# Kernel optimization log

Measured on AMD Instinct MI355X. Metric: run time of the kernel, lower is better.

The kernel has to match this reference:

```python
import jax, jax.numpy as jnp
import numpy as np


def gin_layer(x, src, dst, ew, w1, b1, w2, b2):
    # message: gather source features, scale by edge weight  [E, d]
    msg = x[src] * ew[:, None]
    # scatter-add into destination nodes  [N, d]
    agg = jax.ops.segment_sum(msg, dst, num_segments=x.shape[0])
    # GIN update: (1 + eps) * x + aggregate, eps = 0 (default)
    h = agg + x
    # 2-layer MLP (Linear -> ReLU -> Linear, plain last layer)
    h = jax.nn.relu(h @ w1 + b1)
    return h @ w2 + b2


def setup_inputs() -> dict:
    key = jax.random.key(0)
    ks = jax.random.split(key, 16)
    N, E, D = 100000, 1000000, 64
    x = jax.random.normal(ks[0], (N, D), dtype=jnp.float32)
    edge_index = jax.random.randint(ks[1], (2, E), 0, N)
    edge_weight = jax.random.uniform(ks[2], (E,), dtype=jnp.float32)

    def lin(k, fi, fo):
        return jax.random.normal(k, (fi, fo), dtype=jnp.float32) * (1.0 / np.sqrt(fi))

    return {
        "x": x, "edge_index": edge_index, "edge_weight": edge_weight,
        "w11": lin(ks[3], 64, 64),  "b11": jnp.zeros(64, jnp.float32),
        "w12": lin(ks[4], 64, 64),  "b12": jnp.zeros(64, jnp.float32),
        "w21": lin(ks[5], 64, 128), "b21": jnp.zeros(128, jnp.float32),
        "w22": lin(ks[6], 128, 64), "b22": jnp.zeros(64, jnp.float32),
        "w31": lin(ks[7], 64, 64),  "b31": jnp.zeros(64, jnp.float32),
        "w32": lin(ks[8], 64, 64),  "b32": jnp.zeros(64, jnp.float32),
    }


def reference(x, edge_index, edge_weight,
              w11, b11, w12, b12,
              w21, b21, w22, b22,
              w31, b31, w32, b32):
    src, dst = edge_index[0], edge_index[1]
    # dropout is identity in eval mode
    h = gin_layer(x, src, dst, edge_weight, w11, b11, w12, b12)
    h = jax.nn.relu(h)
    h = gin_layer(h, src, dst, edge_weight, w21, b21, w22, b22)
    h = jax.nn.relu(h)
    h = gin_layer(h, src, dst, edge_weight, w31, b31, w32, b32)
    return h
```

## Files before the change

kernel.cpp:

```cpp
#include <hip/hip_runtime.h>
#include <math.h>


#define FEAT  64
#define BINW  128
#define BSH   7
#define NBLK  256
#define SRCB  25
#define PADSLACK 2048

typedef __attribute__((ext_vector_type(8))) short bfrag;
typedef __attribute__((ext_vector_type(4))) float ffrag;
typedef __attribute__((ext_vector_type(2))) float f32x2;

__device__ __forceinline__ unsigned short f2bf_rne(float x) {
    union { float f; unsigned u; } v; v.f = x;
    unsigned r = (v.u + 0x7fffu + ((v.u >> 16) & 1u)) >> 16;
    return (unsigned short)r;
}
__device__ __forceinline__ float bf2f(unsigned short h) {
    union { unsigned u; float f; } v; v.u = ((unsigned)h) << 16;
    return v.f;
}
__device__ __forceinline__ f32x2 bf2x2(unsigned d) {
    f32x2 r;
    r.x = __uint_as_float(d << 16);
    r.y = __uint_as_float(d & 0xffff0000u);
    return r;
}
__device__ __forceinline__ unsigned cvt_pk_bf16(float a, float b) {
    unsigned r;
    asm("v_cvt_pk_bf16_f32 %0, %1, %2" : "=v"(r) : "v"(a), "v"(b));
    return r;
}
__device__ __forceinline__ void split8(const float u[8], bfrag& hi, bfrag& lo) {
    union { unsigned d[4]; bfrag b; } ch, cl;
#pragma unroll
    for (int i = 0; i < 4; ++i) {
        unsigned h = cvt_pk_bf16(u[2*i], u[2*i+1]);
        float f0 = __uint_as_float(h << 16);
        float f1 = __uint_as_float(h & 0xffff0000u);
        ch.d[i] = h;
        cl.d[i] = cvt_pk_bf16(u[2*i] - f0, u[2*i+1] - f1);
    }
    hi = ch.b; lo = cl.b;
}

__device__ __forceinline__ void pack_one(const float* __restrict__ w,
                                         unsigned short* __restrict__ hi,
                                         unsigned short* __restrict__ lo,
                                         int K, int Hc, int i) {
    int KF = K >> 5;
    int j    = i & 7;
    int lane = (i >> 3) & 63;
    int fb   = i >> 9;
    int kf   = fb % KF;
    int cg   = fb / KF;
    int k    = kf * 32 + ((lane >> 4) << 3) + j;
    int col  = cg * 16 + (lane & 15);
    float x = w[k * Hc + col];
    unsigned short h = f2bf_rne(x);
    hi[i] = h;
    lo[i] = f2bf_rne(x - bf2f(h));
}

__global__ __launch_bounds__(256)
void k_pre(const float4* __restrict__ x4, ushort4* __restrict__ xb4,
           int n4, int gCvt,
           const int* __restrict__ dst, int* __restrict__ counts,
           int E, int NBINS,
           const float* w11, const float* w12, const float* w21,
           const float* w22, const float* w31, const float* w32,
           unsigned short* p11h, unsigned short* p11l,
           unsigned short* p12h, unsigned short* p12l,
           unsigned short* p21h, unsigned short* p21l,
           unsigned short* p22h, unsigned short* p22l,
           unsigned short* p31h, unsigned short* p31l,
           unsigned short* p32h, unsigned short* p32l) {
    __shared__ int h[1024];
    const int bb = blockIdx.x, tid = threadIdx.x;
    if (bb < gCvt) {
        int i = bb * 256 + tid;
        if (i < n4) {
            float4 v = x4[i];
            ushort4 o;
            o.x = f2bf_rne(v.x); o.y = f2bf_rne(v.y);
            o.z = f2bf_rne(v.z); o.w = f2bf_rne(v.w);
            xb4[i] = o;
        }
    } else if (bb < gCvt + NBLK) {
        const int b = bb - gCvt;
        for (int i = tid; i < NBINS; i += 256) h[i] = 0;
        __syncthreads();
        const int chunk = (E + NBLK - 1) / NBLK;
        const int ebeg = b * chunk;
        const int eend = (ebeg + chunk < E) ? ebeg + chunk : E;
        for (int e = ebeg + tid; e < eend; e += 256)
            atomicAdd(&h[dst[e] >> BSH], 1);
        __syncthreads();
        for (int i = tid; i < NBINS; i += 256)
            counts[i * NBLK + b] = h[i];
    } else {
        int i = (bb - gCvt - NBLK) * 256 + tid;
        if      (i <  4096) pack_one(w11, p11h, p11l,  64,  64, i);
        else if (i <  8192) pack_one(w12, p12h, p12l,  64,  64, i - 4096);
        else if (i < 16384) pack_one(w21, p21h, p21l,  64, 128, i - 8192);
        else if (i < 24576) pack_one(w22, p22h, p22l, 128,  64, i - 16384);
        else if (i < 28672) pack_one(w31, p31h, p31l,  64,  64, i - 24576);
        else                pack_one(w32, p32h, p32l,  64,  64, i - 28672);
    }
}

__global__ __launch_bounds__(256)
void k_scanA2(int* __restrict__ counts, int* __restrict__ bintotal, int NBINS) {
    __shared__ int tmp[256];
    const int bin = blockIdx.x, tid = threadIdx.x;
    int c = counts[bin * NBLK + tid];
    tmp[tid] = c;
    __syncthreads();
    for (int off = 1; off < 256; off <<= 1) {
        int t = (tid >= off) ? tmp[tid - off] : 0;
        __syncthreads();
        tmp[tid] += t;
        __syncthreads();
    }
    counts[bin * NBLK + tid] = tmp[tid] - c;
    if (tid == 255) bintotal[bin] = tmp[255];
}

__global__ __launch_bounds__(256)
void k_place2(const int* __restrict__ src, const int* __restrict__ dst,
              const float* __restrict__ ew, const int* __restrict__ counts,
              const int* __restrict__ bintotal, int* __restrict__ binstart,
              int2* __restrict__ binbuf, int E, int NBINS) {
    __shared__ int bs[1024];
    __shared__ int tmp[256];
    __shared__ int base[1024];
    const int b = blockIdx.x, tid = threadIdx.x;

    int v[4]; int s = 0;
#pragma unroll
    for (int j = 0; j < 4; ++j) {
        int idx = tid * 4 + j;
        v[j] = (idx < NBINS) ? bintotal[idx] : 0;
        s += v[j];
    }
    tmp[tid] = s;
    __syncthreads();
    for (int off = 1; off < 256; off <<= 1) {
        int t = (tid >= off) ? tmp[tid - off] : 0;
        __syncthreads();
        tmp[tid] += t;
        __syncthreads();
    }
    int run = tmp[tid] - s;
#pragma unroll
    for (int j = 0; j < 4; ++j) {
        bs[tid * 4 + j] = run;
        run += v[j];
    }
    __syncthreads();

    if (b == 0) {
        for (int i = tid; i < NBINS; i += 256) binstart[i] = bs[i];
        if (tid == 0) binstart[NBINS] = E;
    }

    for (int i = tid; i < NBINS; i += 256)
        base[i] = bs[i] + counts[i * NBLK + b];
    __syncthreads();

    const int chunk = (E + NBLK - 1) / NBLK;
    const int ebeg = b * chunk;
    const int eend = (ebeg + chunk < E) ? ebeg + chunk : E;
    for (int e = ebeg + tid; e < eend; e += 256) {
        int d = dst[e];
        int slot = atomicAdd(&base[d >> BSH], 1);
        int key = ((d & (BINW - 1)) << SRCB) | src[e];
        binbuf[slot] = make_int2(key, __float_as_int(ew[e]));
    }
}

__global__ __launch_bounds__(256)
void k_binsort(const int2* __restrict__ binbuf, const int* __restrict__ binstart,
               int* __restrict__ pbeg, int* __restrict__ pend,
               int2* __restrict__ csr_pad, int N) {
    __shared__ int cnt[BINW];
    __shared__ int cur[BINW];
    __shared__ int pex[BINW];
    const int b    = blockIdx.x;
    const int base = binstart[b];
    const int ne   = binstart[b + 1] - base;
    const int tid  = threadIdx.x;
    const int base_pad = ((base + 15) & ~15) + b * PADSLACK;

    if (tid < BINW) cnt[tid] = 0;
    __syncthreads();
    for (int i = tid; i < ne; i += 256)
        atomicAdd(&cnt[(binbuf[base + i].x >> SRCB) & (BINW - 1)], 1);
    __syncthreads();
    int pc = 0;
    if (tid < BINW) {
        int c = cnt[tid];
        pc = c ? ((c + 15) & ~15) : 16;
        cur[tid] = pc;
    }
    __syncthreads();
    for (int off = 1; off < BINW; off <<= 1) {
        int v = (tid < BINW && tid >= off) ? cur[tid - off] : 0;
        __syncthreads();
        if (tid < BINW) cur[tid] += v;
        __syncthreads();
    }
    if (tid < BINW) {
        int ex = cur[tid] - pc;
        pex[tid] = ex;
        int node = b * BINW + tid;
        if (node < N) {
            pbeg[node] = base_pad + ex;
            pend[node] = base_pad + ex + pc;
        }
        cur[tid] = 0;
    }
    __syncthreads();
    for (int i = tid; i < ne; i += 256) {
        int2 e = binbuf[base + i];
        int dl = (e.x >> SRCB) & (BINW - 1);
        int r = atomicAdd(&cur[dl], 1);
        csr_pad[base_pad + pex[dl] + r] =
            make_int2((e.x & ((1 << SRCB) - 1)) << 7, e.y);
    }
    __syncthreads();
    if (tid < BINW) {
        int c = cnt[tid];
        int pcn = c ? ((c + 15) & ~15) : 16;
        int o = base_pad + pex[tid];
        for (int j = c; j < pcn; ++j)
            csr_pad[o + j] = make_int2(0, 0);
    }
}

template<int H, bool RELU_OUT, bool OUT_BF16>
__global__ __launch_bounds__(256)
void k_fused(const ushort* __restrict__ in, void* __restrict__ outv,
             const int* __restrict__ pbeg, const int* __restrict__ pend,
             const int2* __restrict__ csr_pad,
             const unsigned short* __restrict__ w1h, const unsigned short* __restrict__ w1l,
             const float* __restrict__ b1,
             const unsigned short* __restrict__ w2h, const unsigned short* __restrict__ w2l,
             const float* __restrict__ b2, int N) {
    constexpr int SH   = H + 4;
    constexpr int CG1  = H / 16;
    constexpr int CGH1 = CG1 / 4;
    constexpr int KF2  = H / 32;
    __shared__ float hs[16 * SH];

    const int t = threadIdx.x;
    const int wk = t >> 6, lane = t & 63;
    const int m = lane & 15, q = lane >> 4;
    const int m8 = m * 8;
    const int tnode0 = blockIdx.x * 16;
    float* hw = hs;
    const char* inB = reinterpret_cast<const char*>(in);
    const int4* csr4 = reinterpret_cast<const int4*>(csr_pad);

    const int gnode = tnode0 + wk * 4 + q;
    const int beg = pbeg[gnode];
    const int end = pend[gnode];
    uint2 xr = *reinterpret_cast<const uint2*>(inB + (size_t)gnode * 128 + m8);

    {
        const int nl = wk * 4 + q;
        f32x2 acc01 = {0.f, 0.f};
        f32x2 acc23 = {0.f, 0.f};
        for (int p = beg; p < end; p += 16) {
            int4 e2[8];
#pragma unroll
            for (int u = 0; u < 8; ++u)
                e2[u] = csr4[(p >> 1) + u];
            uint2 v2[16];
#pragma unroll
            for (int u = 0; u < 8; ++u) {
                v2[2*u]   = *reinterpret_cast<const uint2*>(inB + (unsigned)e2[u].x + m8);
                v2[2*u+1] = *reinterpret_cast<const uint2*>(inB + (unsigned)e2[u].z + m8);
            }
#pragma unroll
            for (int u = 0; u < 8; ++u) {
                f32x2 w0 = {__int_as_float(e2[u].y), __int_as_float(e2[u].y)};
                f32x2 w1 = {__int_as_float(e2[u].w), __int_as_float(e2[u].w)};
                acc01 = __builtin_elementwise_fma(w0, bf2x2(v2[2*u].x),   acc01);
                acc23 = __builtin_elementwise_fma(w0, bf2x2(v2[2*u].y),   acc23);
                acc01 = __builtin_elementwise_fma(w1, bf2x2(v2[2*u+1].x), acc01);
                acc23 = __builtin_elementwise_fma(w1, bf2x2(v2[2*u+1].y), acc23);
            }
        }
        acc01 = acc01 + bf2x2(xr.x);
        acc23 = acc23 + bf2x2(xr.y);
        float4 accv = make_float4(acc01.x, acc01.y, acc23.x, acc23.y);
        *reinterpret_cast<float4*>(&hw[nl * SH + m * 4]) = accv;
    }
    __syncthreads();

    const bfrag* w1hp = reinterpret_cast<const bfrag*>(w1h);
    const bfrag* w1lp = reinterpret_cast<const bfrag*>(w1l);
    const bfrag* w2hp = reinterpret_cast<const bfrag*>(w2h);
    const bfrag* w2lp = reinterpret_cast<const bfrag*>(w2l);

    bfrag ah[2], al[2];
#pragma unroll
    for (int kf = 0; kf < 2; ++kf) {
        const float* base = &hw[m * SH + kf * 32 + q * 8];
        float4 u0 = *reinterpret_cast<const float4*>(base);
        float4 u1 = *reinterpret_cast<const float4*>(base + 4);
        float u[8] = {u0.x, u0.y, u0.z, u0.w, u1.x, u1.y, u1.z, u1.w};
        split8(u, ah[kf], al[kf]);
    }
    __syncthreads();

    __builtin_amdgcn_s_setprio(1);
#pragma unroll
    for (int cgi = 0; cgi < CGH1; ++cgi) {
        const int cg = wk * CGH1 + cgi;
        ffrag c = {0.f, 0.f, 0.f, 0.f};
#pragma unroll
        for (int kf = 0; kf < 2; ++kf) {
            bfrag bh = w1hp[(cg * 2 + kf) * 64 + lane];
            bfrag bl = w1lp[(cg * 2 + kf) * 64 + lane];
            c = __builtin_amdgcn_mfma_f32_16x16x32_bf16(ah[kf], bh, c, 0, 0, 0);
            c = __builtin_amdgcn_mfma_f32_16x16x32_bf16(al[kf], bh, c, 0, 0, 0);
            c = __builtin_amdgcn_mfma_f32_16x16x32_bf16(ah[kf], bl, c, 0, 0, 0);
        }
        float bias = b1[cg * 16 + m];
#pragma unroll
        for (int r = 0; r < 4; ++r) {
            float hv = fmaxf(c[r] + bias, 0.f);
            hw[(q * 4 + r) * SH + cg * 16 + m] = hv;
        }
    }
    __builtin_amdgcn_s_setprio(0);
    __syncthreads();

    bfrag gh[KF2], gl[KF2];
#pragma unroll
    for (int kf = 0; kf < KF2; ++kf) {
        const float* base = &hw[m * SH + kf * 32 + q * 8];
        float4 u0 = *reinterpret_cast<const float4*>(base);
        float4 u1 = *reinterpret_cast<const float4*>(base + 4);
        float u[8] = {u0.x, u0.y, u0.z, u0.w, u1.x, u1.y, u1.z, u1.w};
        split8(u, gh[kf], gl[kf]);
    }

    {
        const int cg = wk;
        ffrag c = {0.f, 0.f, 0.f, 0.f};
        __builtin_amdgcn_s_setprio(1);
#pragma unroll
        for (int kf = 0; kf < KF2; ++kf) {
            bfrag bh = w2hp[(cg * KF2 + kf) * 64 + lane];
            bfrag bl = w2lp[(cg * KF2 + kf) * 64 + lane];
            c = __builtin_amdgcn_mfma_f32_16x16x32_bf16(gh[kf], bh, c, 0, 0, 0);
            c = __builtin_amdgcn_mfma_f32_16x16x32_bf16(gl[kf], bh, c, 0, 0, 0);
            c = __builtin_amdgcn_mfma_f32_16x16x32_bf16(gh[kf], bl, c, 0, 0, 0);
        }
        __builtin_amdgcn_s_setprio(0);
        float bias = b2[cg * 16 + m];
#pragma unroll
        for (int r = 0; r < 4; ++r) {
            int nd = tnode0 + q * 4 + r;
            float v = c[r] + bias;
            if (RELU_OUT) v = fmaxf(v, 0.f);
            if (OUT_BF16)
                ((unsigned short*)outv)[(size_t)nd * FEAT + cg * 16 + m] = f2bf_rne(v);
            else
                ((float*)outv)[(size_t)nd * FEAT + cg * 16 + m] = v;
        }
    }
}

extern "C" void kernel_launch(void* const* d_in, const int* in_sizes, int n_in,
                              void* d_out, int out_size, void* d_ws, size_t ws_size,
                              hipStream_t stream) {
    const float* x   = (const float*)d_in[0];
    const int*   ei  = (const int*)  d_in[1];
    const float* ew  = (const float*)d_in[2];
    const float* w11 = (const float*)d_in[3];
    const float* b11 = (const float*)d_in[4];
    const float* w12 = (const float*)d_in[5];
    const float* b12 = (const float*)d_in[6];
    const float* w21 = (const float*)d_in[7];
    const float* b21 = (const float*)d_in[8];
    const float* w22 = (const float*)d_in[9];
    const float* b22 = (const float*)d_in[10];
    const float* w31 = (const float*)d_in[11];
    const float* b31 = (const float*)d_in[12];
    const float* w32 = (const float*)d_in[13];
    const float* b32 = (const float*)d_in[14];

    const int N = in_sizes[0] / FEAT;
    const int E = in_sizes[2];
    const int* srci = ei;
    const int* dsti = ei + E;
    const int NBINS = (N + BINW - 1) >> BSH;

    unsigned short* xb0 = (unsigned short*)d_ws;
    unsigned short* xb1 = xb0 + (size_t)N * FEAT;
    int*   pbeg     = (int*)(xb1 + (size_t)N * FEAT);
    int*   pend     = pbeg + N;
    int*   counts   = pend + N;
    int*   bintotal = counts + NBINS * NBLK;
    int*   binstart = bintotal + NBINS;
    size_t a16 = ((size_t)(binstart + NBINS + 1) + 15) & ~(size_t)15;
    int2*  binbuf   = (int2*)a16;
    int2*  csr_pad  = (int2*)(binbuf + E);
    size_t pk = (size_t)(csr_pad + E + (size_t)NBINS * PADSLACK + 1024);
    unsigned short* p11h = (unsigned short*)pk;
    unsigned short* p11l = p11h + 4096;
    unsigned short* p12h = p11l + 4096;
    unsigned short* p12l = p12h + 4096;
    unsigned short* p21h = p12l + 4096;
    unsigned short* p21l = p21h + 8192;
    unsigned short* p22h = p21l + 8192;
    unsigned short* p22l = p22h + 8192;
    unsigned short* p31h = p22l + 8192;
    unsigned short* p31l = p31h + 4096;
    unsigned short* p32h = p31l + 4096;
    unsigned short* p32l = p32h + 4096;
    float* outF = (float*)d_out;

    const int n4   = N * 16;
    const int gCvt = (n4 + 255) / 256;
    const int gMlp = (N + 15) / 16;
    const int gPre = gCvt + NBLK + 128;

    k_pre<<<gPre, 256, 0, stream>>>((const float4*)x, (ushort4*)xb0, n4, gCvt,
                                    dsti, counts, E, NBINS,
                                    w11, w12, w21, w22, w31, w32,
                                    p11h, p11l, p12h, p12l, p21h, p21l,
                                    p22h, p22l, p31h, p31l, p32h, p32l);
    k_scanA2 <<<NBINS, 256, 0, stream>>>(counts, bintotal, NBINS);
    k_place2 <<<NBLK,  256, 0, stream>>>(srci, dsti, ew, counts, bintotal,
                                         binstart, binbuf, E, NBINS);
    k_binsort<<<NBINS, 256, 0, stream>>>(binbuf, binstart, pbeg, pend,
                                         csr_pad, N);

    k_fused<64,  true,  true ><<<gMlp, 256, 0, stream>>>(xb0, xb1, pbeg, pend, csr_pad,
                                                         p11h, p11l, b11, p12h, p12l, b12, N);
    k_fused<128, true,  true ><<<gMlp, 256, 0, stream>>>(xb1, xb0, pbeg, pend, csr_pad,
                                                         p21h, p21l, b21, p22h, p22l, b22, N);
    k_fused<64,  false, false><<<gMlp, 256, 0, stream>>>(xb0, outF, pbeg, pend, csr_pad,
                                                         p31h, p31l, b31, p32h, p32l, b32, N);
}
```

Baseline: 257.8 us.

## Split CSR into fixed first-16 slots per node plus overflow buffer

Replaces the padded per-node CSR (pbeg/pend arrays) with a fixed 16-edge slot per node stored contiguously by node index, plus a per-bin overflow region for nodes with more than 16 edges and a packed int2 header. The fused gather kernel now loads the first 16 edges unconditionally at a node-computable address and loops over overflow only when needed. This removes the dependent load of begin/end before edge fetch and most loop control. It also splits the shared buffer into separate accumulator and hidden arrays so one __syncthreads can be dropped. The cost is a larger first16 array (N*16 entries, mostly zero-padded given avg degree 10), so more bytes are read per node.

```diff
diff --git a/kernel.cpp b/kernel.cpp
--- a/kernel.cpp
+++ b/kernel.cpp
@@ -7,7 +7,7 @@
 #define BSH   7
 #define NBLK  256
 #define SRCB  25
-#define PADSLACK 2048
+#define OVFSLACK 2048
 
 typedef __attribute__((ext_vector_type(8))) short bfrag;
 typedef __attribute__((ext_vector_type(4))) float ffrag;
@@ -183,27 +183,27 @@
 
 __global__ __launch_bounds__(256)
 void k_binsort(const int2* __restrict__ binbuf, const int* __restrict__ binstart,
-               int* __restrict__ pbeg, int* __restrict__ pend,
-               int2* __restrict__ csr_pad, int N) {
+               int2* __restrict__ hdr, int2* __restrict__ first16,
+               int2* __restrict__ ovfbuf, int N) {
     __shared__ int cnt[BINW];
     __shared__ int cur[BINW];
-    __shared__ int pex[BINW];
+    __shared__ int oex[BINW];
     const int b    = blockIdx.x;
     const int base = binstart[b];
     const int ne   = binstart[b + 1] - base;
     const int tid  = threadIdx.x;
-    const int base_pad = ((base + 15) & ~15) + b * PADSLACK;
+    const int obase = b * OVFSLACK;
 
     if (tid < BINW) cnt[tid] = 0;
     __syncthreads();
     for (int i = tid; i < ne; i += 256)
         atomicAdd(&cnt[(binbuf[base + i].x >> SRCB) & (BINW - 1)], 1);
     __syncthreads();
-    int pc = 0;
+    int opc = 0;
     if (tid < BINW) {
         int c = cnt[tid];
-        pc = c ? ((c + 15) & ~15) : 16;
-        cur[tid] = pc;
+        opc = (c > 16) ? ((c - 16 + 15) & ~15) : 0;
+        cur[tid] = opc;
     }
     __syncthreads();
     for (int off = 1; off < BINW; off <<= 1) {
@@ -213,13 +213,10 @@
         __syncthreads();
     }
     if (tid < BINW) {
-        int ex = cur[tid] - pc;
-        pex[tid] = ex;
+        int ex = cur[tid] - opc;
+        oex[tid] = ex;
         int node = b * BINW + tid;
-        if (node < N) {
-            pbeg[node] = base_pad + ex;
-            pend[node] = base_pad + ex + pc;
-        }
+        if (node < N) hdr[node] = make_int2(obase + ex, opc);
         cur[tid] = 0;
     }
     __syncthreads();
@@ -227,57 +224,88 @@
         int2 e = binbuf[base + i];
         int dl = (e.x >> SRCB) & (BINW - 1);
         int r = atomicAdd(&cur[dl], 1);
-        csr_pad[base_pad + pex[dl] + r] =
-            make_int2((e.x & ((1 << SRCB) - 1)) << 7, e.y);
+        int2 out = make_int2((e.x & ((1 << SRCB) - 1)) << 7, e.y);
+        int node = b * BINW + dl;
+        if (r < 16) first16[(size_t)node * 16 + r] = out;
+        else        ovfbuf[obase + oex[dl] + (r - 16)] = out;
     }
     __syncthreads();
     if (tid < BINW) {
         int c = cnt[tid];
-        int pcn = c ? ((c + 15) & ~15) : 16;
-        int o = base_pad + pex[tid];
-        for (int j = c; j < pcn; ++j)
-            csr_pad[o + j] = make_int2(0, 0);
+        int node = b * BINW + tid;
+        if (node < N) {
+            for (int j = c; j < 16; ++j)
+                first16[(size_t)node * 16 + j] = make_int2(0, 0);
+            int opcn = (c > 16) ? ((c - 16 + 15) & ~15) : 0;
+            if (opcn > 0) {
+                int o = obase + oex[tid];
+                for (int j = c - 16; j < opcn; ++j)
+                    ovfbuf[o + j] = make_int2(0, 0);
+            }
+        }
     }
 }
 
 template<int H, bool RELU_OUT, bool OUT_BF16>
 __global__ __launch_bounds__(256)
 void k_fused(const ushort* __restrict__ in, void* __restrict__ outv,
-             const int* __restrict__ pbeg, const int* __restrict__ pend,
-             const int2* __restrict__ csr_pad,
+             const int2* __restrict__ hdr, const int2* __restrict__ first16,
+             const int2* __restrict__ ovfbuf,
              const unsigned short* __restrict__ w1h, const unsigned short* __restrict__ w1l,
              const float* __restrict__ b1,
              const unsigned short* __restrict__ w2h, const unsigned short* __restrict__ w2l,
              const float* __restrict__ b2, int N) {
-    constexpr int SH   = H + 4;
+    constexpr int SA   = 68;
+    constexpr int SH1  = H + 4;
     constexpr int CG1  = H / 16;
     constexpr int CGH1 = CG1 / 4;
     constexpr int KF2  = H / 32;
-    __shared__ float hs[16 * SH];
+    __shared__ float hs_acc[16 * SA];
+    __shared__ float hs_h[16 * SH1];
 
     const int t = threadIdx.x;
     const int wk = t >> 6, lane = t & 63;
     const int m = lane & 15, q = lane >> 4;
     const int m8 = m * 8;
     const int tnode0 = blockIdx.x * 16;
-    float* hw = hs;
     const char* inB = reinterpret_cast<const char*>(in);
-    const int4* csr4 = reinterpret_cast<const int4*>(csr_pad);
 
     const int gnode = tnode0 + wk * 4 + q;
-    const int beg = pbeg[gnode];
-    const int end = pend[gnode];
+    const int2 hd = hdr[gnode];
     uint2 xr = *reinterpret_cast<const uint2*>(inB + (size_t)gnode * 128 + m8);
+    const int4* f16 = reinterpret_cast<const int4*>(first16) + (size_t)gnode * 8;
+
+    f32x2 acc01 = {0.f, 0.f};
+    f32x2 acc23 = {0.f, 0.f};
 
     {
-        const int nl = wk * 4 + q;
-        f32x2 acc01 = {0.f, 0.f};
-        f32x2 acc23 = {0.f, 0.f};
-        for (int p = beg; p < end; p += 16) {
+        int4 e2[8];
+#pragma unroll
+        for (int u = 0; u < 8; ++u)
+            e2[u] = f16[u];
+        uint2 v2[16];
+#pragma unroll
+        for (int u = 0; u < 8; ++u) {
+            v2[2*u]   = *reinterpret_cast<const uint2*>(inB + (unsigned)e2[u].x + m8);
+            v2[2*u+1] = *reinterpret_cast<const uint2*>(inB + (unsigned)e2[u].z + m8);
+        }
+#pragma unroll
+        for (int u = 0; u < 8; ++u) {
+            f32x2 w0 = {__int_as_float(e2[u].y), __int_as_float(e2[u].y)};
+            f32x2 w1 = {__int_as_float(e2[u].w), __int_as_float(e2[u].w)};
+            acc01 = __builtin_elementwise_fma(w0, bf2x2(v2[2*u].x),   acc01);
+            acc23 = __builtin_elementwise_fma(w0, bf2x2(v2[2*u].y),   acc23);
+            acc01 = __builtin_elementwise_fma(w1, bf2x2(v2[2*u+1].x), acc01);
+            acc23 = __builtin_elementwise_fma(w1, bf2x2(v2[2*u+1].y), acc23);
+        }
+    }
+    if (hd.y > 0) {
+        const int4* ovf4 = reinterpret_cast<const int4*>(ovfbuf);
+        for (int p = hd.x; p < hd.x + hd.y; p += 16) {
             int4 e2[8];
 #pragma unroll
             for (int u = 0; u < 8; ++u)
-                e2[u] = csr4[(p >> 1) + u];
+                e2[u] = ovf4[(p >> 1) + u];
             uint2 v2[16];
 #pragma unroll
             for (int u = 0; u < 8; ++u) {
@@ -294,10 +322,13 @@
                 acc23 = __builtin_elementwise_fma(w1, bf2x2(v2[2*u+1].y), acc23);
             }
         }
-        acc01 = acc01 + bf2x2(xr.x);
-        acc23 = acc23 + bf2x2(xr.y);
+    }
+    acc01 = acc01 + bf2x2(xr.x);
+    acc23 = acc23 + bf2x2(xr.y);
+    {
+        const int nl = wk * 4 + q;
         float4 accv = make_float4(acc01.x, acc01.y, acc23.x, acc23.y);
-        *reinterpret_cast<float4*>(&hw[nl * SH + m * 4]) = accv;
+        *reinterpret_cast<float4*>(&hs_acc[nl * SA + m * 4]) = accv;
     }
     __syncthreads();
 
@@ -309,13 +340,12 @@
     bfrag ah[2], al[2];
 #pragma unroll
     for (int kf = 0; kf < 2; ++kf) {
-        const float* base = &hw[m * SH + kf * 32 + q * 8];
+        const float* base = &hs_acc[m * SA + kf * 32 + q * 8];
         float4 u0 = *reinterpret_cast<const float4*>(base);
         float4 u1 = *reinterpret_cast<const float4*>(base + 4);
         float u[8] = {u0.x, u0.y, u0.z, u0.w, u1.x, u1.y, u1.z, u1.w};
         split8(u, ah[kf], al[kf]);
     }
-    __syncthreads();
 
     __builtin_amdgcn_s_setprio(1);
 #pragma unroll
@@ -334,7 +364,7 @@
 #pragma unroll
         for (int r = 0; r < 4; ++r) {
             float hv = fmaxf(c[r] + bias, 0.f);
-            hw[(q * 4 + r) * SH + cg * 16 + m] = hv;
+            hs_h[(q * 4 + r) * SH1 + cg * 16 + m] = hv;
         }
     }
     __builtin_amdgcn_s_setprio(0);
@@ -343,7 +373,7 @@
     bfrag gh[KF2], gl[KF2];
 #pragma unroll
     for (int kf = 0; kf < KF2; ++kf) {
-        const float* base = &hw[m * SH + kf * 32 + q * 8];
+        const float* base = &hs_h[m * SH1 + kf * 32 + q * 8];
         float4 u0 = *reinterpret_cast<const float4*>(base);
         float4 u1 = *reinterpret_cast<const float4*>(base + 4);
         float u[8] = {u0.x, u0.y, u0.z, u0.w, u1.x, u1.y, u1.z, u1.w};
@@ -404,15 +434,15 @@
 
     unsigned short* xb0 = (unsigned short*)d_ws;
     unsigned short* xb1 = xb0 + (size_t)N * FEAT;
-    int*   pbeg     = (int*)(xb1 + (size_t)N * FEAT);
-    int*   pend     = pbeg + N;
-    int*   counts   = pend + N;
+    int2*  hdr      = (int2*)(xb1 + (size_t)N * FEAT);
+    int2*  first16  = hdr + N;
+    int*   counts   = (int*)(first16 + (size_t)N * 16);
     int*   bintotal = counts + NBINS * NBLK;
     int*   binstart = bintotal + NBINS;
     size_t a16 = ((size_t)(binstart + NBINS + 1) + 15) & ~(size_t)15;
     int2*  binbuf   = (int2*)a16;
-    int2*  csr_pad  = (int2*)(binbuf + E);
-    size_t pk = (size_t)(csr_pad + E + (size_t)NBINS * PADSLACK + 1024);
+    int2*  ovfbuf   = binbuf + E;
+    size_t pk = (size_t)(ovfbuf + (size_t)NBINS * OVFSLACK);
     unsigned short* p11h = (unsigned short*)pk;
     unsigned short* p11l = p11h + 4096;
     unsigned short* p12h = p11l + 4096;
@@ -440,13 +470,13 @@
     k_scanA2 <<<NBINS, 256, 0, stream>>>(counts, bintotal, NBINS);
     k_place2 <<<NBLK,  256, 0, stream>>>(srci, dsti, ew, counts, bintotal,
                                          binstart, binbuf, E, NBINS);
-    k_binsort<<<NBINS, 256, 0, stream>>>(binbuf, binstart, pbeg, pend,
-                                         csr_pad, N);
-
-    k_fused<64,  true,  true ><<<gMlp, 256, 0, stream>>>(xb0, xb1, pbeg, pend, csr_pad,
+    k_binsort<<<NBINS, 256, 0, stream>>>(binbuf, binstart, hdr, first16,
+                                         ovfbuf, N);
+
+    k_fused<64,  true,  true ><<<gMlp, 256, 0, stream>>>(xb0, xb1, hdr, first16, ovfbuf,
                                                          p11h, p11l, b11, p12h, p12l, b12, N);
-    k_fused<128, true,  true ><<<gMlp, 256, 0, stream>>>(xb1, xb0, pbeg, pend, csr_pad,
+    k_fused<128, true,  true ><<<gMlp, 256, 0, stream>>>(xb1, xb0, hdr, first16, ovfbuf,
                                                          p21h, p21l, b21, p22h, p22l, b22, N);
-    k_fused<64,  false, false><<<gMlp, 256, 0, stream>>>(xb0, outF, pbeg, pend, csr_pad,
+    k_fused<64,  false, false><<<gMlp, 256, 0, stream>>>(xb0, outF, hdr, first16, ovfbuf,
                                                          p31h, p31l, b31, p32h, p32l, b32, N);
 }
```

Result: no change. 252.8 us (-1.9%).
